# Kernel tuning notes

Hardware: AMD Instinct MI355X
Metric: run time of the kernel (lower is better)

Reference implementation:

```python
import jax, jax.numpy as jnp
import numpy as np

N_NODES = 100000
N_EDGES = 600000
D_IN = 128
D_HID = 128
D_OUT = 128


def setup_inputs() -> dict:
    key = jax.random.key(0)
    k = jax.random.split(key, 6)
    x = jax.random.normal(k[0], (N_NODES, D_IN), dtype=jnp.float32)
    edge_index = jax.random.randint(k[1], (2, N_EDGES), 0, N_NODES, dtype=jnp.int64)
    # GCNConv params: glorot-ish weights, zero-init biases (randn-scaled here)
    W1 = jax.random.normal(k[2], (D_IN, D_HID), dtype=jnp.float32) / np.sqrt(D_IN)
    b1 = jnp.zeros((D_HID,), dtype=jnp.float32)
    W2 = jax.random.normal(k[3], (D_HID, D_OUT), dtype=jnp.float32) / np.sqrt(D_HID)
    b2 = jnp.zeros((D_OUT,), dtype=jnp.float32)
    return {"x": x, "edge_index": edge_index, "W1": W1, "b1": b1, "W2": W2, "b2": b2}


def _gcn_conv(x, W, b, src, dst, deg_inv_sqrt, n_nodes):
    # PyG GCNConv: h = x @ W; out_i = sum_{j->i} d_j^{-1/2} d_i^{-1/2} h_j + b
    h = x @ W  # [N, Dout]
    norm = (deg_inv_sqrt[src] * deg_inv_sqrt[dst])[:, None]  # [E, 1]
    msg = h[src] * norm  # gather: [E, Dout]
    out = jax.ops.segment_sum(msg, dst, num_segments=n_nodes)  # scatter-add
    return out + b


def reference(x, edge_index, W1, b1, W2, b2):
    n = x.shape[0]
    # add self loops
    loops = jnp.arange(n, dtype=edge_index.dtype)
    src = jnp.concatenate([edge_index[0], loops])
    dst = jnp.concatenate([edge_index[1], loops])
    # symmetric normalization degrees (computed on dst, deg >= 1 due to self loops)
    deg = jax.ops.segment_sum(jnp.ones_like(dst, dtype=x.dtype), dst, num_segments=n)
    deg_inv_sqrt = jax.lax.rsqrt(deg)
    h = _gcn_conv(x, W1, b1, src, dst, deg_inv_sqrt, n)
    h = jax.nn.relu(h)  # dropout is identity in eval mode
    out = _gcn_conv(h, W2, b2, src, dst, deg_inv_sqrt, n)
    return out
```

## Files before the change

kernel.cpp:

```cpp
#include <hip/hip_runtime.h>

#define D 128

typedef __attribute__((ext_vector_type(8))) short bf16x8;
typedef __attribute__((ext_vector_type(4))) float f32x4;
typedef __attribute__((ext_vector_type(4))) unsigned u32x4;

__device__ inline unsigned short f2bf(float f) {
    unsigned u = __builtin_bit_cast(unsigned, f);
    u += 0x7FFFu + ((u >> 16) & 1u);
    return (unsigned short)(u >> 16);
}
__device__ inline float bf_lo(unsigned u) { return __builtin_bit_cast(float, u << 16); }
__device__ inline float bf_hi(unsigned u) { return __builtin_bit_cast(float, u & 0xFFFF0000u); }

__global__ void k_zero1(int* __restrict__ a, int n) {
    int i = blockIdx.x * blockDim.x + threadIdx.x;
    if (i < n) a[i] = 0;
}

__global__ void k_hist_rank(const int* __restrict__ dst, int* __restrict__ counts,
                            int* __restrict__ rank, int nE) {
    int e4 = (blockIdx.x * blockDim.x + threadIdx.x) * 4;
    if (e4 + 4 <= nE) {
        const int4 d = *reinterpret_cast<const int4*>(dst + e4);
        int4 r;
        r.x = atomicAdd(&counts[d.x], 1);
        r.y = atomicAdd(&counts[d.y], 1);
        r.z = atomicAdd(&counts[d.z], 1);
        r.w = atomicAdd(&counts[d.w], 1);
        *reinterpret_cast<int4*>(rank + e4) = r;
    } else {
        for (int e = e4; e < nE; ++e) rank[e] = atomicAdd(&counts[dst[e]], 1);
    }
}

__global__ __launch_bounds__(256) void k_scan_part(const int* __restrict__ counts,
                                                   int* __restrict__ bsum,
                                                   float* __restrict__ dis, int n) {
    const int t = threadIdx.x;
    const int base = blockIdx.x * 1024 + t * 4;
    int4 c = make_int4(0, 0, 0, 0);
    if (base + 4 <= n) {
        c = *reinterpret_cast<const int4*>(counts + base);
        float4 dv;
        dv.x = rsqrtf((float)(c.x + 1));
        dv.y = rsqrtf((float)(c.y + 1));
        dv.z = rsqrtf((float)(c.z + 1));
        dv.w = rsqrtf((float)(c.w + 1));
        *reinterpret_cast<float4*>(dis + base) = dv;
    } else if (base < n) {
        int cc[4] = {0, 0, 0, 0};
        for (int k = 0; k < 4; ++k)
            if (base + k < n) {
                cc[k] = counts[base + k];
                dis[base + k] = rsqrtf((float)(cc[k] + 1));
            }
        c.x = cc[0]; c.y = cc[1]; c.z = cc[2]; c.w = cc[3];
    }
    __shared__ int red[256];
    red[t] = c.x + c.y + c.z + c.w;
    __syncthreads();
    for (int off = 128; off > 0; off >>= 1) {
        if (t < off) red[t] += red[t + off];
        __syncthreads();
    }
    if (t == 0) bsum[blockIdx.x] = red[0];
}

__global__ __launch_bounds__(256) void k_scan_final(const int* __restrict__ counts,
                                                    const int* __restrict__ bsum,
                                                    int* __restrict__ starts, int n, int nB) {
    __shared__ int sb[128];
    __shared__ int ts[256];
    const int t = threadIdx.x;
    const int b = blockIdx.x;

    if (t < 128) sb[t] = (t < nB) ? bsum[t] : 0;
    __syncthreads();
    for (int off = 1; off < 128; off <<= 1) {
        int add = (t < 128 && t >= off) ? sb[t - off] : 0;
        __syncthreads();
        if (t < 128) sb[t] += add;
        __syncthreads();
    }
    const int block_off = (b > 0) ? sb[b - 1] : 0;

    const int base = b * 1024 + t * 4;
    int4 c = make_int4(0, 0, 0, 0);
    if (base + 4 <= n) {
        c = *reinterpret_cast<const int4*>(counts + base);
    } else if (base < n) {
        if (base + 0 < n) c.x = counts[base + 0];
        if (base + 1 < n) c.y = counts[base + 1];
        if (base + 2 < n) c.z = counts[base + 2];
    }
    const int s = c.x + c.y + c.z + c.w;
    ts[t] = s;
    __syncthreads();
    for (int off = 1; off < 256; off <<= 1) {
        int add = (t >= off) ? ts[t - off] : 0;
        __syncthreads();
        ts[t] += add;
        __syncthreads();
    }
    int excl = block_off + ts[t] - s;

    int4 w;
    w.x = excl;
    w.y = w.x + c.x;
    w.z = w.y + c.y;
    w.w = w.z + c.z;
    if (base + 4 <= n) {
        *reinterpret_cast<int4*>(starts + base) = w;
    } else if (base < n) {
        if (base + 0 < n) starts[base + 0] = w.x;
        if (base + 1 < n) starts[base + 1] = w.y;
        if (base + 2 < n) starts[base + 2] = w.z;
    }
    if (b == 0 && t == 0) starts[n] = sb[nB - 1];
}

__global__ void k_scatter_nr(const int* __restrict__ src, const int* __restrict__ dst,
                             const int* __restrict__ rank, const int* __restrict__ starts,
                             int* __restrict__ esrc, int nE) {
    int e4 = (blockIdx.x * blockDim.x + threadIdx.x) * 4;
    if (e4 + 4 <= nE) {
        const int4 s = *reinterpret_cast<const int4*>(src + e4);
        const int4 d = *reinterpret_cast<const int4*>(dst + e4);
        const int4 r = *reinterpret_cast<const int4*>(rank + e4);
        esrc[starts[d.x] + r.x] = s.x;
        esrc[starts[d.y] + r.y] = s.y;
        esrc[starts[d.z] + r.z] = s.z;
        esrc[starts[d.w] + r.w] = s.w;
    } else {
        for (int e = e4; e < nE; ++e)
            esrc[starts[dst[e]] + rank[e]] = src[e];
    }
}

__global__ __launch_bounds__(256) void k_pack_w(const float* __restrict__ W,
                                                unsigned short* __restrict__ wp) {
    const int t = blockIdx.x * blockDim.x + threadIdx.x;
    const int lane = t & 63;
    const int frag = t >> 6;
    const int ct = frag >> 2;
    const int kk = frag & 3;
    const int col16 = lane & 15;
    const int kgrp = lane >> 4;
    bf16x8 d;
#pragma unroll
    for (int e = 0; e < 8; ++e)
        d[e] = (short)f2bf(W[(kk * 32 + kgrp * 8 + e) * D + ct * 16 + col16]);
    *reinterpret_cast<bf16x8*>(wp + (size_t)t * 8) = d;
}

template <bool IN_BF16, bool RELU>
__global__ __launch_bounds__(256, 2) void k_gemm_mfma(const void* __restrict__ Xv,
                                                      const unsigned short* __restrict__ wp,
                                                      const float* __restrict__ dis,
                                                      unsigned short* __restrict__ outbf,
                                                      int n) {
    __shared__ __align__(16) unsigned short At[64 * 128];
    const int tid = threadIdx.x;
    const int lane = tid & 63;
    const int wv = tid >> 6;
    const int col16 = lane & 15;
    const int kgrp = lane >> 4;
    const int st = blockIdx.x;

    float4 pf[8];
    bf16x8 pb[4];
#pragma unroll
    for (int c = 0; c < 4; ++c) {
        const int idx = c * 2048 + tid * 8;
        const int row = idx >> 7;
        const int col = idx & 127;
        int grow = st * 64 + row;
        if (grow >= n) grow = n - 1;
        if constexpr (IN_BF16) {
            pb[c] = *reinterpret_cast<const bf16x8*>(
                    (const unsigned short*)Xv + (size_t)grow * D + col);
        } else {
            const float4* p = reinterpret_cast<const float4*>(
                    (const float*)Xv + (size_t)grow * D + col);
            pf[2 * c] = p[0];
            pf[2 * c + 1] = p[1];
        }
    }

    bf16x8 bw[8][4];
#pragma unroll
    for (int ct = 0; ct < 8; ++ct)
#pragma unroll
        for (int kk = 0; kk < 4; ++kk)
            bw[ct][kk] = *reinterpret_cast<const bf16x8*>(
                    wp + (size_t)((ct * 4 + kk) * 64 + lane) * 8);

#pragma unroll
    for (int c = 0; c < 4; ++c) {
        const int idx = c * 2048 + tid * 8;
        const int row = idx >> 7;
        const int col = idx & 127;
        bf16x8 d;
        if constexpr (IN_BF16) {
            d = pb[c];
            if (RELU) {
#pragma unroll
                for (int e = 0; e < 8; ++e)
                    d[e] = (short)((d[e] & (short)0x8000) ? 0 : d[e]);
            }
        } else {
            const float4 f0 = pf[2 * c], f1 = pf[2 * c + 1];
            float v[8] = {f0.x, f0.y, f0.z, f0.w, f1.x, f1.y, f1.z, f1.w};
#pragma unroll
            for (int e = 0; e < 8; ++e) {
                float f = v[e];
                if (RELU) f = fmaxf(f, 0.0f);
                d[e] = (short)f2bf(f);
            }
        }
        const int waddr = row * 128 + (col ^ ((row & 7) << 3));
        *reinterpret_cast<bf16x8*>(&At[waddr]) = d;
    }
    __syncthreads();

    bf16x8 a[4];
#pragma unroll
    for (int kk = 0; kk < 4; ++kk) {
        const int raddr = (wv * 16 + col16) * 128 +
                          ((kk * 32 + kgrp * 8) ^ ((col16 & 7) << 3));
        a[kk] = *reinterpret_cast<const bf16x8*>(&At[raddr]);
    }

    f32x4 acc[8];
#pragma unroll
    for (int ct = 0; ct < 8; ++ct) acc[ct] = (f32x4){0.f, 0.f, 0.f, 0.f};
#pragma unroll
    for (int kk = 0; kk < 4; ++kk)
#pragma unroll
        for (int ct = 0; ct < 8; ++ct)
            acc[ct] = __builtin_amdgcn_mfma_f32_16x16x32_bf16(bw[ct][kk], a[kk], acc[ct], 0, 0, 0);

    const int node = st * 64 + wv * 16 + col16;
    if (node < n) {
        const float dn = dis[node];
        unsigned short* op = outbf + (size_t)node * D + kgrp * 4;
#pragma unroll
        for (int ct = 0; ct < 8; ++ct) {
            uint2 w;
            w.x = (unsigned)f2bf(dn * acc[ct][0]) | ((unsigned)f2bf(dn * acc[ct][1]) << 16);
            w.y = (unsigned)f2bf(dn * acc[ct][2]) | ((unsigned)f2bf(dn * acc[ct][3]) << 16);
            *reinterpret_cast<uint2*>(op + ct * 16) = w;
        }
    }
}

template <bool OUT_BF16>
__global__ __launch_bounds__(256) void k_gather_agg(const unsigned short* __restrict__ hs,
                                                    const int* __restrict__ starts,
                                                    const int* __restrict__ esrc,
                                                    const float* __restrict__ dis,
                                                    const float* __restrict__ b,
                                                    void* __restrict__ outv, int n) {
    const int lane = threadIdx.x & 63;
    const int wv = threadIdx.x >> 6;
    const int grp = lane >> 4;
    const int sub = lane & 15;
    const int i = (blockIdx.x * 4 + wv) * 4 + grp;
    const bool active = (i < n);
    const int ic = active ? i : (n - 1);

    const float di = dis[ic];
    const int beg = starts[ic];
    const int end = starts[ic + 1];

    auto row16 = [&](int s) -> u32x4 {
        return *reinterpret_cast<const u32x4*>(hs + (size_t)s * D + sub * 8);
    };

    float acc[8];
    {
        const u32x4 u = row16(ic);
#pragma unroll
        for (int e = 0; e < 4; ++e) {
            acc[2 * e] = bf_lo(u[e]);
            acc[2 * e + 1] = bf_hi(u[e]);
        }
    }

#define ACCUM(u)                              \
    _Pragma("unroll") for (int e = 0; e < 4; ++e) { \
        acc[2 * e] += bf_lo((u)[e]);          \
        acc[2 * e + 1] += bf_hi((u)[e]);      \
    }

    int j = beg;
    while (j < end) {
        const int cnt = min(end - j, 16);
        const int myedge = (sub < cnt) ? esrc[j + sub] : 0;
        int k = 0;
        for (; k + 4 <= cnt; k += 4) {
            const int s0 = __shfl(myedge, (grp << 4) | (k + 0));
            const int s1 = __shfl(myedge, (grp << 4) | (k + 1));
            const int s2 = __shfl(myedge, (grp << 4) | (k + 2));
            const int s3 = __shfl(myedge, (grp << 4) | (k + 3));
            const u32x4 u0 = row16(s0);
            const u32x4 u1 = row16(s1);
            const u32x4 u2 = row16(s2);
            const u32x4 u3 = row16(s3);
            ACCUM(u0) ACCUM(u1) ACCUM(u2) ACCUM(u3)
        }
        for (; k < cnt; ++k) {
            const int s0 = __shfl(myedge, (grp << 4) | k);
            const u32x4 u0 = row16(s0);
            ACCUM(u0)
        }
        j += 16;
    }
#undef ACCUM

    if (!active) return;

    const float4 bv0 = reinterpret_cast<const float4*>(b)[sub * 2 + 0];
    const float4 bv1 = reinterpret_cast<const float4*>(b)[sub * 2 + 1];
    float o[8];
    o[0] = di * acc[0] + bv0.x; o[1] = di * acc[1] + bv0.y;
    o[2] = di * acc[2] + bv0.z; o[3] = di * acc[3] + bv0.w;
    o[4] = di * acc[4] + bv1.x; o[5] = di * acc[5] + bv1.y;
    o[6] = di * acc[6] + bv1.z; o[7] = di * acc[7] + bv1.w;

    if constexpr (OUT_BF16) {
        u32x4 w;
#pragma unroll
        for (int e = 0; e < 4; ++e)
            w[e] = (unsigned)f2bf(o[2 * e]) | ((unsigned)f2bf(o[2 * e + 1]) << 16);
        *reinterpret_cast<u32x4*>((unsigned short*)outv + (size_t)i * D + sub * 8) = w;
    } else {
        float4* op = reinterpret_cast<float4*>((float*)outv + (size_t)i * D + sub * 8);
        op[0] = make_float4(o[0], o[1], o[2], o[3]);
        op[1] = make_float4(o[4], o[5], o[6], o[7]);
    }
}

extern "C" void kernel_launch(void* const* d_in, const int* in_sizes, int n_in,
                              void* d_out, int out_size, void* d_ws, size_t ws_size,
                              hipStream_t stream) {
    const float* x  = (const float*)d_in[0];
    const int*   ei = (const int*)d_in[1];
    const float* W1 = (const float*)d_in[2];
    const float* b1 = (const float*)d_in[3];
    const float* W2 = (const float*)d_in[4];
    const float* b2 = (const float*)d_in[5];
    float* out = (float*)d_out;

    const int n  = in_sizes[0] / D;
    const int nE = in_sizes[1] / 2;
    const int* src = ei;
    const int* dst = ei + nE;

    char* ws = (char*)d_ws;
    float*          dis    = (float*)(ws);
    int*            counts = (int*)(ws + (1ull  << 19));
    int*            starts = (int*)(ws + (2ull  << 19));
    int*            esrc   = (int*)(ws + (4ull  << 19));
    int*            bsum   = (int*)(ws + (6ull  << 20));
    unsigned short* hs_bf  = (unsigned short*)(ws + (8ull  << 20));
    int*            rank   = (int*)(ws + (34ull << 20));
    unsigned short* wp1    = (unsigned short*)(ws + (37ull << 20));
    unsigned short* wp2    = (unsigned short*)(ws + (37ull << 20) + (1ull << 15));
    unsigned short* agg_bf = (unsigned short*)(ws + (40ull << 20));

    const int B = 256;
    const int gn = (n + B - 1) / B;
    const int ge4 = (nE + B * 4 - 1) / (B * 4);
    const int nB = (n + 1023) / 1024;

    k_pack_w<<<8, B, 0, stream>>>(W1, wp1);
    k_pack_w<<<8, B, 0, stream>>>(W2, wp2);

    k_zero1<<<gn, B, 0, stream>>>(counts, n);
    k_hist_rank<<<ge4, B, 0, stream>>>(dst, counts, rank, nE);
    k_scan_part<<<nB, B, 0, stream>>>(counts, bsum, dis, n);
    k_scan_final<<<nB, B, 0, stream>>>(counts, bsum, starts, n, nB);
    k_scatter_nr<<<ge4, B, 0, stream>>>(src, dst, rank, starts, esrc, nE);

    const int nst = (n + 63) / 64;
    const int agg_grid = (n + 15) / 16;

    k_gemm_mfma<false, false><<<nst, B, 0, stream>>>(x, wp1, dis, hs_bf, n);
    k_gather_agg<true><<<agg_grid, B, 0, stream>>>(hs_bf, starts, esrc, dis, b1, agg_bf, n);

    k_gemm_mfma<true, true><<<nst, B, 0, stream>>>(agg_bf, wp2, dis, hs_bf, n);
    k_gather_agg<false><<<agg_grid, B, 0, stream>>>(hs_bf, starts, esrc, dis, b2, out, n);
}
```

Measured before the change: 158.0 us.

## Fuse layer-1 aggregation with layer-2 GEMM and deepen gather unrolling

Merges the first gather-aggregate with the second MFMA GEMM into one kernel: each block aggregates 64 node rows, applies bias and ReLU, stores them as bf16 in LDS and multiplies by W2. This removes the intermediate bf16 aggregate round-trip through global memory and one launch. The GEMM now loads W fragments in two halves so occupancy can rise to 3 blocks per CU, the gather issues 8 row loads per batch instead of 4, and both weight packs run in a single launch. The fused kernel processes four rows per wave serially, so it may lose some memory-level parallelism in the gather phase.

```diff
diff --git a/kernel.cpp b/kernel.cpp
--- a/kernel.cpp
+++ b/kernel.cpp
@@ -139,11 +139,14 @@
     }
 }
 
-__global__ __launch_bounds__(256) void k_pack_w(const float* __restrict__ W,
-                                                unsigned short* __restrict__ wp) {
+__global__ __launch_bounds__(256) void k_pack_w2(const float* __restrict__ W1,
+                                                 const float* __restrict__ W2,
+                                                 unsigned short* __restrict__ wp) {
     const int t = blockIdx.x * blockDim.x + threadIdx.x;
-    const int lane = t & 63;
-    const int frag = t >> 6;
+    const float* W = (t < 2048) ? W1 : W2;
+    const int tt = t & 2047;
+    const int lane = tt & 63;
+    const int frag = tt >> 6;
     const int ct = frag >> 2;
     const int kk = frag & 3;
     const int col16 = lane & 15;
@@ -155,8 +158,51 @@
     *reinterpret_cast<bf16x8*>(wp + (size_t)t * 8) = d;
 }
 
+__device__ __forceinline__ void gather_rows(const unsigned short* __restrict__ hs,
+                                            const int* __restrict__ esrc,
+                                            int beg, int end, int grp, int sub, int ic,
+                                            float acc[8]) {
+    auto row16 = [&](int s) -> u32x4 {
+        return *reinterpret_cast<const u32x4*>(hs + (size_t)s * D + sub * 8);
+    };
+    {
+        const u32x4 u = row16(ic);
+#pragma unroll
+        for (int e = 0; e < 4; ++e) {
+            acc[2 * e] = bf_lo(u[e]);
+            acc[2 * e + 1] = bf_hi(u[e]);
+        }
+    }
+    int j = beg;
+    while (j < end) {
+        const int cnt = min(end - j, 16);
+        const int myedge = (sub < cnt) ? esrc[j + sub] : 0;
+        for (int k = 0; k < cnt; k += 8) {
+            u32x4 u[8];
+#pragma unroll
+            for (int q = 0; q < 8; ++q) {
+                const int tq = min(k + q, cnt - 1);
+                const int s = __shfl(myedge, (grp << 4) | tq);
+                u[q] = row16(s);
+            }
+            const int rem = cnt - k;
+#pragma unroll
+            for (int q = 0; q < 8; ++q) {
+                if (q < rem) {
+#pragma unroll
+                    for (int e = 0; e < 4; ++e) {
+                        acc[2 * e] += bf_lo(u[q][e]);
+                        acc[2 * e + 1] += bf_hi(u[q][e]);
+                    }
+                }
+            }
+        }
+        j += 16;
+    }
+}
+
 template <bool IN_BF16, bool RELU>
-__global__ __launch_bounds__(256, 2) void k_gemm_mfma(const void* __restrict__ Xv,
+__global__ __launch_bounds__(256, 3) void k_gemm_mfma(const void* __restrict__ Xv,
                                                       const unsigned short* __restrict__ wp,
                                                       const float* __restrict__ dis,
                                                       unsigned short* __restrict__ outbf,
@@ -189,14 +235,6 @@
         }
     }
 
-    bf16x8 bw[8][4];
-#pragma unroll
-    for (int ct = 0; ct < 8; ++ct)
-#pragma unroll
-        for (int kk = 0; kk < 4; ++kk)
-            bw[ct][kk] = *reinterpret_cast<const bf16x8*>(
-                    wp + (size_t)((ct * 4 + kk) * 64 + lane) * 8);
-
 #pragma unroll
     for (int c = 0; c < 4; ++c) {
         const int idx = c * 2048 + tid * 8;
@@ -233,36 +271,136 @@
         a[kk] = *reinterpret_cast<const bf16x8*>(&At[raddr]);
     }
 
-    f32x4 acc[8];
-#pragma unroll
-    for (int ct = 0; ct < 8; ++ct) acc[ct] = (f32x4){0.f, 0.f, 0.f, 0.f};
-#pragma unroll
-    for (int kk = 0; kk < 4; ++kk)
-#pragma unroll
-        for (int ct = 0; ct < 8; ++ct)
-            acc[ct] = __builtin_amdgcn_mfma_f32_16x16x32_bf16(bw[ct][kk], a[kk], acc[ct], 0, 0, 0);
-
     const int node = st * 64 + wv * 16 + col16;
-    if (node < n) {
-        const float dn = dis[node];
-        unsigned short* op = outbf + (size_t)node * D + kgrp * 4;
-#pragma unroll
-        for (int ct = 0; ct < 8; ++ct) {
-            uint2 w;
-            w.x = (unsigned)f2bf(dn * acc[ct][0]) | ((unsigned)f2bf(dn * acc[ct][1]) << 16);
-            w.y = (unsigned)f2bf(dn * acc[ct][2]) | ((unsigned)f2bf(dn * acc[ct][3]) << 16);
-            *reinterpret_cast<uint2*>(op + ct * 16) = w;
-        }
-    }
-}
-
-template <bool OUT_BF16>
+    const float dn = (node < n) ? dis[node] : 0.0f;
+    unsigned short* op = outbf + (size_t)node * D + kgrp * 4;
+
+#pragma unroll
+    for (int h = 0; h < 2; ++h) {
+        bf16x8 bw[4][4];
+#pragma unroll
+        for (int c2 = 0; c2 < 4; ++c2)
+#pragma unroll
+            for (int kk = 0; kk < 4; ++kk)
+                bw[c2][kk] = *reinterpret_cast<const bf16x8*>(
+                        wp + (size_t)(((h * 4 + c2) * 4 + kk) * 64 + lane) * 8);
+
+        f32x4 acc[4];
+#pragma unroll
+        for (int c2 = 0; c2 < 4; ++c2) acc[c2] = (f32x4){0.f, 0.f, 0.f, 0.f};
+#pragma unroll
+        for (int kk = 0; kk < 4; ++kk)
+#pragma unroll
+            for (int c2 = 0; c2 < 4; ++c2)
+                acc[c2] = __builtin_amdgcn_mfma_f32_16x16x32_bf16(bw[c2][kk], a[kk], acc[c2], 0, 0, 0);
+
+        if (node < n) {
+#pragma unroll
+            for (int c2 = 0; c2 < 4; ++c2) {
+                uint2 w;
+                w.x = (unsigned)f2bf(dn * acc[c2][0]) | ((unsigned)f2bf(dn * acc[c2][1]) << 16);
+                w.y = (unsigned)f2bf(dn * acc[c2][2]) | ((unsigned)f2bf(dn * acc[c2][3]) << 16);
+                *reinterpret_cast<uint2*>(op + (h * 4 + c2) * 16) = w;
+            }
+        }
+    }
+}
+
+__global__ __launch_bounds__(256, 3) void k_gather_gemm(const unsigned short* __restrict__ hs,
+                                                        const int* __restrict__ starts,
+                                                        const int* __restrict__ esrc,
+                                                        const float* __restrict__ dis,
+                                                        const float* __restrict__ bias,
+                                                        const unsigned short* __restrict__ wp,
+                                                        unsigned short* __restrict__ outbf,
+                                                        int n) {
+    __shared__ __align__(16) unsigned short At[64 * 128];
+    const int tid = threadIdx.x;
+    const int lane = tid & 63;
+    const int wv = tid >> 6;
+    const int col16 = lane & 15;
+    const int kgrp = lane >> 4;
+    const int grp = lane >> 4;
+    const int sub = lane & 15;
+    const int st = blockIdx.x;
+
+    const float4 bv0 = reinterpret_cast<const float4*>(bias)[sub * 2 + 0];
+    const float4 bv1 = reinterpret_cast<const float4*>(bias)[sub * 2 + 1];
+
+#pragma unroll 1
+    for (int p = 0; p < 4; ++p) {
+        const int lrow = wv * 16 + p * 4 + grp;
+        const int i = st * 64 + lrow;
+        const int ic = (i < n) ? i : (n - 1);
+        const float di = dis[ic];
+        float acc[8];
+        gather_rows(hs, esrc, starts[ic], starts[ic + 1], grp, sub, ic, acc);
+
+        float o[8];
+        o[0] = di * acc[0] + bv0.x; o[1] = di * acc[1] + bv0.y;
+        o[2] = di * acc[2] + bv0.z; o[3] = di * acc[3] + bv0.w;
+        o[4] = di * acc[4] + bv1.x; o[5] = di * acc[5] + bv1.y;
+        o[6] = di * acc[6] + bv1.z; o[7] = di * acc[7] + bv1.w;
+
+        u32x4 w;
+#pragma unroll
+        for (int e = 0; e < 4; ++e)
+            w[e] = (unsigned)f2bf(fmaxf(o[2 * e], 0.0f)) |
+                   ((unsigned)f2bf(fmaxf(o[2 * e + 1], 0.0f)) << 16);
+        const int waddr = lrow * 128 + ((sub * 8) ^ ((lrow & 7) << 3));
+        *reinterpret_cast<u32x4*>(&At[waddr]) = w;
+    }
+    __syncthreads();
+
+    bf16x8 a[4];
+#pragma unroll
+    for (int kk = 0; kk < 4; ++kk) {
+        const int raddr = (wv * 16 + col16) * 128 +
+                          ((kk * 32 + kgrp * 8) ^ ((col16 & 7) << 3));
+        a[kk] = *reinterpret_cast<const bf16x8*>(&At[raddr]);
+    }
+
+    const int node = st * 64 + wv * 16 + col16;
+    const float dn = (node < n) ? dis[node] : 0.0f;
+    unsigned short* op = outbf + (size_t)node * D + kgrp * 4;
+
+#pragma unroll
+    for (int h = 0; h < 2; ++h) {
+        bf16x8 bw[4][4];
+#pragma unroll
+        for (int c2 = 0; c2 < 4; ++c2)
+#pragma unroll
+            for (int kk = 0; kk < 4; ++kk)
+                bw[c2][kk] = *reinterpret_cast<const bf16x8*>(
+                        wp + (size_t)(((h * 4 + c2) * 4 + kk) * 64 + lane) * 8);
+
+        f32x4 acc[4];
+#pragma unroll
+        for (int c2 = 0; c2 < 4; ++c2) acc[c2] = (f32x4){0.f, 0.f, 0.f, 0.f};
+#pragma unroll
+        for (int kk = 0; kk < 4; ++kk)
+#pragma unroll
+            for (int c2 = 0; c2 < 4; ++c2)
+                acc[c2] = __builtin_amdgcn_mfma_f32_16x16x32_bf16(bw[c2][kk], a[kk], acc[c2], 0, 0, 0);
+
+        if (node < n) {
+#pragma unroll
+            for (int c2 = 0; c2 < 4; ++c2) {
+                uint2 w;
+                w.x = (unsigned)f2bf(dn * acc[c2][0]) | ((unsigned)f2bf(dn * acc[c2][1]) << 16);
+                w.y = (unsigned)f2bf(dn * acc[c2][2]) | ((unsigned)f2bf(dn * acc[c2][3]) << 16);
+                *reinterpret_cast<uint2*>(op + (h * 4 + c2) * 16) = w;
+            }
+        }
+    }
+}
+
 __global__ __launch_bounds__(256) void k_gather_agg(const unsigned short* __restrict__ hs,
                                                     const int* __restrict__ starts,
                                                     const int* __restrict__ esrc,
                                                     const float* __restrict__ dis,
                                                     const float* __restrict__ b,
-                                                    void* __restrict__ outv, int n) {
+                                                    float* __restrict__ outv, int n) {
     const int lane = threadIdx.x & 63;
     const int wv = threadIdx.x >> 6;
     const int grp = lane >> 4;
@@ -272,75 +410,18 @@
     const int ic = active ? i : (n - 1);
 
     const float di = dis[ic];
-    const int beg = starts[ic];
-    const int end = starts[ic + 1];
-
-    auto row16 = [&](int s) -> u32x4 {
-        return *reinterpret_cast<const u32x4*>(hs + (size_t)s * D + sub * 8);
-    };
-
     float acc[8];
-    {
-        const u32x4 u = row16(ic);
-#pragma unroll
-        for (int e = 0; e < 4; ++e) {
-            acc[2 * e] = bf_lo(u[e]);
-            acc[2 * e + 1] = bf_hi(u[e]);
-        }
-    }
-
-#define ACCUM(u)                              \
-    _Pragma("unroll") for (int e = 0; e < 4; ++e) { \
-        acc[2 * e] += bf_lo((u)[e]);          \
-        acc[2 * e + 1] += bf_hi((u)[e]);      \
-    }
-
-    int j = beg;
-    while (j < end) {
-        const int cnt = min(end - j, 16);
-        const int myedge = (sub < cnt) ? esrc[j + sub] : 0;
-        int k = 0;
-        for (; k + 4 <= cnt; k += 4) {
-            const int s0 = __shfl(myedge, (grp << 4) | (k + 0));
-            const int s1 = __shfl(myedge, (grp << 4) | (k + 1));
-            const int s2 = __shfl(myedge, (grp << 4) | (k + 2));
-            const int s3 = __shfl(myedge, (grp << 4) | (k + 3));
-            const u32x4 u0 = row16(s0);
-            const u32x4 u1 = row16(s1);
-            const u32x4 u2 = row16(s2);
-            const u32x4 u3 = row16(s3);
-            ACCUM(u0) ACCUM(u1) ACCUM(u2) ACCUM(u3)
-        }
-        for (; k < cnt; ++k) {
-            const int s0 = __shfl(myedge, (grp << 4) | k);
-            const u32x4 u0 = row16(s0);
-            ACCUM(u0)
-        }
-        j += 16;
-    }
-#undef ACCUM
+    gather_rows(hs, esrc, starts[ic], starts[ic + 1], grp, sub, ic, acc);
 
     if (!active) return;
 
     const float4 bv0 = reinterpret_cast<const float4*>(b)[sub * 2 + 0];
     const float4 bv1 = reinterpret_cast<const float4*>(b)[sub * 2 + 1];
-    float o[8];
-    o[0] = di * acc[0] + bv0.x; o[1] = di * acc[1] + bv0.y;
-    o[2] = di * acc[2] + bv0.z; o[3] = di * acc[3] + bv0.w;
-    o[4] = di * acc[4] + bv1.x; o[5] = di * acc[5] + bv1.y;
-    o[6] = di * acc[6] + bv1.z; o[7] = di * acc[7] + bv1.w;
-
-    if constexpr (OUT_BF16) {
-        u32x4 w;
-#pragma unroll
-        for (int e = 0; e < 4; ++e)
-            w[e] = (unsigned)f2bf(o[2 * e]) | ((unsigned)f2bf(o[2 * e + 1]) << 16);
-        *reinterpret_cast<u32x4*>((unsigned short*)outv + (size_t)i * D + sub * 8) = w;
-    } else {
-        float4* op = reinterpret_cast<float4*>((float*)outv + (size_t)i * D + sub * 8);
-        op[0] = make_float4(o[0], o[1], o[2], o[3]);
-        op[1] = make_float4(o[4], o[5], o[6], o[7]);
-    }
+    float4* op = reinterpret_cast<float4*>(outv + (size_t)i * D + sub * 8);
+    op[0] = make_float4(di * acc[0] + bv0.x, di * acc[1] + bv0.y,
+                        di * acc[2] + bv0.z, di * acc[3] + bv0.w);
+    op[1] = make_float4(di * acc[4] + bv1.x, di * acc[5] + bv1.y,
+                        di * acc[6] + bv1.z, di * acc[7] + bv1.w);
 }
 
 extern "C" void kernel_launch(void* const* d_in, const int* in_sizes, int n_in,
@@ -367,17 +448,18 @@
     int*            bsum   = (int*)(ws + (6ull  << 20));
     unsigned short* hs_bf  = (unsigned short*)(ws + (8ull  << 20));
     int*            rank   = (int*)(ws + (34ull << 20));
-    unsigned short* wp1    = (unsigned short*)(ws + (37ull << 20));
-    unsigned short* wp2    = (unsigned short*)(ws + (37ull << 20) + (1ull << 15));
-    unsigned short* agg_bf = (unsigned short*)(ws + (40ull << 20));
+    unsigned short* wp     = (unsigned short*)(ws + (37ull << 20));
+    unsigned short* hs2_bf = (unsigned short*)(ws + (40ull << 20));
+
+    unsigned short* wp1 = wp;
+    unsigned short* wp2 = wp + 2048 * 8;
 
     const int B = 256;
     const int gn = (n + B - 1) / B;
     const int ge4 = (nE + B * 4 - 1) / (B * 4);
     const int nB = (n + 1023) / 1024;
 
-    k_pack_w<<<8, B, 0, stream>>>(W1, wp1);
-    k_pack_w<<<8, B, 0, stream>>>(W2, wp2);
+    k_pack_w2<<<16, B, 0, stream>>>(W1, W2, wp);
 
     k_zero1<<<gn, B, 0, stream>>>(counts, n);
     k_hist_rank<<<ge4, B, 0, stream>>>(dst, counts, rank, nE);
@@ -389,8 +471,6 @@
     const int agg_grid = (n + 15) / 16;
 
     k_gemm_mfma<false, false><<<nst, B, 0, stream>>>(x, wp1, dis, hs_bf, n);
-    k_gather_agg<true><<<agg_grid, B, 0, stream>>>(hs_bf, starts, esrc, dis, b1, agg_bf, n);
-
-    k_gemm_mfma<true, true><<<nst, B, 0, stream>>>(agg_bf, wp2, dis, hs_bf, n);
-    k_gather_agg<false><<<agg_grid, B, 0, stream>>>(hs_bf, starts, esrc, dis, b2, out, n);
-}
+    k_gather_gemm<<<nst, B, 0, stream>>>(hs_bf, starts, esrc, dis, b1, wp2, hs2_bf, n);
+    k_gather_agg<<<agg_grid, B, 0, stream>>>(hs2_bf, starts, esrc, dis, b2, out, n);
+}
```

Measured after the change: 147.7 us. -6.5%, faster.
